# Optimization experiments

Hardware: AMD Instinct MI355X
Metric: run time of the kernel (lower is better)

The kernel has to match this reference:

```python
import jax, jax.numpy as jnp
import numpy as np
import math

B, C, HW = 4, 256, 32          # batch, seq_len (=channels), spatial side
D_MODEL = HW * HW              # 1024
OUT_C = 32 * 32                # 1024
D_STATE = 16
EXPAND = 2
D_INNER = EXPAND * D_MODEL     # 2048
DT_RANK = math.ceil(D_MODEL / 16)  # 64
D_CONV = 4


def setup_inputs() -> dict:
    key = jax.random.key(0)
    ks = jax.random.split(key, 12)
    s = 0.02
    x1 = jax.random.normal(ks[0], (B, C, HW, HW), dtype=jnp.float32)
    in_proj_w = jax.random.normal(ks[1], (2 * D_INNER, D_MODEL), dtype=jnp.float32) * s
    conv_w = jax.random.normal(ks[2], (D_INNER, 1, D_CONV), dtype=jnp.float32) * s
    conv_b = jnp.zeros((D_INNER,), dtype=jnp.float32)
    x_proj_w = jax.random.normal(ks[3], (DT_RANK + 2 * D_STATE, D_INNER), dtype=jnp.float32) * s
    dt_proj_w = jax.random.normal(ks[4], (D_INNER, DT_RANK), dtype=jnp.float32) * s
    dt_proj_b = jnp.zeros((D_INNER,), dtype=jnp.float32)
    A_log = jnp.log(jnp.broadcast_to(jnp.arange(1, D_STATE + 1, dtype=jnp.float32), (D_INNER, D_STATE)))
    D = jnp.ones((D_INNER,), dtype=jnp.float32)
    out_proj_w = jax.random.normal(ks[5], (OUT_C, D_INNER), dtype=jnp.float32) * s
    ln_w = jnp.ones((OUT_C,), dtype=jnp.float32)
    ln_b = jnp.zeros((OUT_C,), dtype=jnp.float32)
    return {"x1": x1, "in_proj_w": in_proj_w, "conv_w": conv_w, "conv_b": conv_b,
            "x_proj_w": x_proj_w, "dt_proj_w": dt_proj_w, "dt_proj_b": dt_proj_b,
            "A_log": A_log, "D": D, "out_proj_w": out_proj_w, "ln_w": ln_w, "ln_b": ln_b}


def _mamba_forward(x, in_proj_w, conv_w, conv_b, x_proj_w, dt_proj_w, dt_proj_b, A_log, D, out_proj_w):
    # x: (B, L, d_model)
    xz = jnp.einsum('bld,ed->ble', x, in_proj_w)            # (B,L,2*d_inner)
    xs, res = jnp.split(xz, 2, axis=-1)                     # each (B,L,d_inner)
    # depthwise causal conv1d, padding=d_conv-1 then truncate to L (== left pad)
    xs_c = jnp.transpose(xs, (0, 2, 1))                     # (B,d_inner,L)
    xs_c = jax.lax.conv_general_dilated(
        xs_c, conv_w, window_strides=(1,), padding=[(D_CONV - 1, 0)],
        dimension_numbers=('NCH', 'OIH', 'NCH'), feature_group_count=D_INNER)
    xs_c = xs_c + conv_b[None, :, None]
    xs = jax.nn.silu(jnp.transpose(xs_c, (0, 2, 1)))        # (B,L,d_inner)
    # input-dependent SSM parameters
    x_dbl = jnp.einsum('bld,ed->ble', xs, x_proj_w)         # (B,L,dt_rank+2N)
    dt, Bm, Cm = jnp.split(x_dbl, [DT_RANK, DT_RANK + D_STATE], axis=-1)
    delta = jax.nn.softplus(jnp.einsum('blr,dr->bld', dt, dt_proj_w) + dt_proj_b)  # (B,L,d_inner)
    A = -jnp.exp(A_log)                                     # (d_inner, N)
    deltaA = jnp.exp(delta[..., None] * A)                  # (B,L,d_inner,N)
    deltaB_u = delta[..., None] * Bm[:, :, None, :] * xs[..., None]  # (B,L,d_inner,N)

    def step(h, inp):
        dA, dBu, Ct = inp                                   # (B,d,N),(B,d,N),(B,N)
        h = dA * h + dBu
        y = jnp.einsum('bdn,bn->bd', h, Ct)
        return h, y

    h0 = jnp.zeros((deltaA.shape[0], D_INNER, D_STATE), dtype=deltaA.dtype)
    _, ys = jax.lax.scan(step, h0, (jnp.transpose(deltaA, (1, 0, 2, 3)),
                                    jnp.transpose(deltaB_u, (1, 0, 2, 3)),
                                    jnp.transpose(Cm, (1, 0, 2))))
    y = jnp.transpose(ys, (1, 0, 2))                        # (B,L,d_inner)
    y = y + D * xs
    y = y * jax.nn.silu(res)
    return jnp.einsum('bld,od->blo', y, out_proj_w)         # (B,L,out_c)


def reference(x1, in_proj_w, conv_w, conv_b, x_proj_w, dt_proj_w, dt_proj_b,
              A_log, D, out_proj_w, ln_w, ln_b):
    b, c, h, w = x1.shape
    x = x1.reshape(b, c, h * w)                             # (B, L=c, d_model)
    y = _mamba_forward(x, in_proj_w, conv_w, conv_b, x_proj_w, dt_proj_w,
                       dt_proj_b, A_log, D, out_proj_w)
    mu = jnp.mean(y, axis=-1, keepdims=True)
    var = jnp.var(y, axis=-1, keepdims=True)
    y = (y - mu) * jax.lax.rsqrt(var + 1e-5) * ln_w + ln_b
    return y.reshape(b, c, 32, 32)
```

## Files before the change

### kernel.cpp

```cpp
#include <hip/hip_runtime.h>
#include <hip/hip_bf16.h>
#include <math.h>

#define BATCH 4
#define SEQL 256
#define DMODEL 1024
#define DINNER 2048
#define DSTATE 16
#define DTRANK 64
#define OUTC 1024
#define NROWS (BATCH * SEQL)
#define NCHUNK 4
#define CH 64

typedef __attribute__((ext_vector_type(8))) short bf16x8;
typedef __attribute__((ext_vector_type(4))) float f32x4;

__global__ __launch_bounds__(256) void gemm_mfma(const __hip_bfloat16* __restrict__ A,
                                                 const __hip_bfloat16* __restrict__ B,
                                                 float* __restrict__ C,
                                                 int M, int N, int K,
                                                 int lda, int ldb) {
    __shared__ __hip_bfloat16 As[2][128 * 32];
    __shared__ __hip_bfloat16 Bs[2][128 * 32];
    const int t  = threadIdx.x;
    const int w  = t >> 6;
    const int ln = t & 63;
    const int wm = w >> 1, wn = w & 1;
    const int q  = ln >> 4, lr = ln & 15;
    const int m0 = blockIdx.y * 128;
    const int n0 = blockIdx.x * 128;
    const int Kpart = K / gridDim.z;
    const int kbase = blockIdx.z * Kpart;

    f32x4 acc[4][4] = {};

    const __hip_bfloat16* Ag = A + (size_t)m0 * lda + kbase;
    const __hip_bfloat16* Bg = B + (size_t)n0 * ldb + kbase;

    auto stage = [&](int k0, int buf) {
        #pragma unroll
        for (int i = 0; i < 2; ++i) {
            const int c = (i * 4 + w) * 64 + ln;
            const int r = c >> 2, col = (c & 3) * 8;
            __builtin_amdgcn_global_load_lds(
                (const __attribute__((address_space(1))) void*)(Ag + (size_t)r * lda + k0 + col),
                (__attribute__((address_space(3))) void*)(As[buf] + (i * 4 + w) * 64 * 8),
                16, 0, 0);
            __builtin_amdgcn_global_load_lds(
                (const __attribute__((address_space(1))) void*)(Bg + (size_t)r * ldb + k0 + col),
                (__attribute__((address_space(3))) void*)(Bs[buf] + (i * 4 + w) * 64 * 8),
                16, 0, 0);
        }
    };

    const int nk = Kpart / 32;
    stage(0, 0);
    __syncthreads();
    for (int kk = 0; kk < nk; ++kk) {
        if (kk + 1 < nk) stage((kk + 1) * 32, (kk + 1) & 1);
        const int buf = kk & 1;
        bf16x8 af[4], bfr[4];
        #pragma unroll
        for (int i = 0; i < 4; ++i)
            af[i] = *(const bf16x8*)(As[buf] + (wm * 64 + i * 16 + lr) * 32 + q * 8);
        #pragma unroll
        for (int j = 0; j < 4; ++j)
            bfr[j] = *(const bf16x8*)(Bs[buf] + (wn * 64 + j * 16 + lr) * 32 + q * 8);
        #pragma unroll
        for (int i = 0; i < 4; ++i)
            #pragma unroll
            for (int j = 0; j < 4; ++j)
                acc[i][j] = __builtin_amdgcn_mfma_f32_16x16x32_bf16(af[i], bfr[j], acc[i][j], 0, 0, 0);
        __syncthreads();
    }
    float* Cz = C + (size_t)blockIdx.z * M * N;
    #pragma unroll
    for (int i = 0; i < 4; ++i) {
        const int mrow = m0 + wm * 64 + i * 16 + q * 4;
        #pragma unroll
        for (int j = 0; j < 4; ++j) {
            const int ncol = n0 + wn * 64 + j * 16 + lr;
            #pragma unroll
            for (int r = 0; r < 4; ++r)
                Cz[(size_t)(mrow + r) * N + ncol] = acc[i][j][r];
        }
    }
}

__global__ __launch_bounds__(256) void gemm_dtsp(const __hip_bfloat16* __restrict__ A,
                                                 const __hip_bfloat16* __restrict__ B,
                                                 const float* __restrict__ bd,
                                                 float* __restrict__ delta) {
    __shared__ __hip_bfloat16 As[128 * 32];
    __shared__ __hip_bfloat16 Bs[128 * 32];
    const int t  = threadIdx.x;
    const int w  = t >> 6;
    const int ln = t & 63;
    const int wm = w >> 1, wn = w & 1;
    const int q  = ln >> 4, lr = ln & 15;
    const int m0 = blockIdx.y * 128;
    const int n0 = blockIdx.x * 128;
    const int lda = 128, ldb = 64, N = 2048;

    f32x4 acc[4][4] = {};
    const __hip_bfloat16* Ag = A + (size_t)m0 * lda;
    const __hip_bfloat16* Bg = B + (size_t)n0 * ldb;

    for (int k0 = 0; k0 < 64; k0 += 32) {
        #pragma unroll
        for (int i = 0; i < 2; ++i) {
            const int c = (i * 4 + w) * 64 + ln;
            const int r = c >> 2, col = (c & 3) * 8;
            __builtin_amdgcn_global_load_lds(
                (const __attribute__((address_space(1))) void*)(Ag + (size_t)r * lda + k0 + col),
                (__attribute__((address_space(3))) void*)(As + (i * 4 + w) * 64 * 8),
                16, 0, 0);
            __builtin_amdgcn_global_load_lds(
                (const __attribute__((address_space(1))) void*)(Bg + (size_t)r * ldb + k0 + col),
                (__attribute__((address_space(3))) void*)(Bs + (i * 4 + w) * 64 * 8),
                16, 0, 0);
        }
        __syncthreads();
        bf16x8 af[4], bfr[4];
        #pragma unroll
        for (int i = 0; i < 4; ++i)
            af[i] = *(const bf16x8*)(As + (wm * 64 + i * 16 + lr) * 32 + q * 8);
        #pragma unroll
        for (int j = 0; j < 4; ++j)
            bfr[j] = *(const bf16x8*)(Bs + (wn * 64 + j * 16 + lr) * 32 + q * 8);
        #pragma unroll
        for (int i = 0; i < 4; ++i)
            #pragma unroll
            for (int j = 0; j < 4; ++j)
                acc[i][j] = __builtin_amdgcn_mfma_f32_16x16x32_bf16(af[i], bfr[j], acc[i][j], 0, 0, 0);
        __syncthreads();
    }
    #pragma unroll
    for (int i = 0; i < 4; ++i) {
        const int mrow = m0 + wm * 64 + i * 16 + q * 4;
        #pragma unroll
        for (int j = 0; j < 4; ++j) {
            const int ncol = n0 + wn * 64 + j * 16 + lr;
            const float bias = bd[ncol];
            #pragma unroll
            for (int r = 0; r < 4; ++r) {
                float v = acc[i][j][r] + bias;
                float sp = (v > 20.f) ? v : log1pf(__expf(v));
                delta[(size_t)(mrow + r) * N + ncol] = sp;
            }
        }
    }
}

__global__ void xdbl_reduce_kernel(const float* __restrict__ part,
                                   float* __restrict__ xdbl,
                                   __hip_bfloat16* __restrict__ xdblb) {
    const int i = blockIdx.x * 256 + threadIdx.x;
    float s = 0.f;
    #pragma unroll
    for (int z = 0; z < 8; ++z) s += part[(size_t)z * (1024 * 128) + i];
    xdbl[i] = s;
    xdblb[i] = __float2bfloat16(s);
}

#define R0 (1024 * 1024)
#define R1 (R0 + 4096 * 1024)
#define R2 (R1 + 2048 * 1024)
#define R3 (R2 + 128 * 2048)
#define R4 (R3 + 2048 * 64)
__global__ void cast_all_kernel(const float* __restrict__ x1,
                                const float* __restrict__ w_in,
                                const float* __restrict__ w_out,
                                const float* __restrict__ w_xp,
                                const float* __restrict__ w_dt,
                                __hip_bfloat16* __restrict__ xa,
                                __hip_bfloat16* __restrict__ wb1,
                                __hip_bfloat16* __restrict__ wob,
                                __hip_bfloat16* __restrict__ wpb,
                                __hip_bfloat16* __restrict__ wdb) {
    int i = blockIdx.x * 256 + threadIdx.x;
    if (i < R0) {
        xa[i] = __float2bfloat16(x1[i]);
    } else if (i < R1) {
        int j = i - R0; wb1[j] = __float2bfloat16(w_in[j]);
    } else if (i < R2) {
        int j = i - R1; wob[j] = __float2bfloat16(w_out[j]);
    } else if (i < R3) {
        int j = i - R2; int e = j >> 11;
        wpb[j] = __float2bfloat16(e < 96 ? w_xp[j] : 0.f);
    } else if (i < R4) {
        int j = i - R3; wdb[j] = __float2bfloat16(w_dt[j]);
    }
}

__global__ void conv_silu_kernel(const float* __restrict__ xz,
                                 const float* __restrict__ conv_w,
                                 const float* __restrict__ conv_b,
                                 float* __restrict__ xs,
                                 __hip_bfloat16* __restrict__ xsb) {
    int idx = blockIdx.x * blockDim.x + threadIdx.x;
    int d = idx & (DINNER - 1);
    int l = (idx >> 11) & (SEQL - 1);
    int b = idx >> 19;
    const float w0 = conv_w[d * 4 + 0];
    const float w1 = conv_w[d * 4 + 1];
    const float w2 = conv_w[d * 4 + 2];
    const float w3 = conv_w[d * 4 + 3];
    float acc = conv_b[d];
    const size_t base = (size_t)(b * SEQL) * (2 * DINNER) + d;
    if (l >= 3) acc += w0 * xz[base + (size_t)(l - 3) * (2 * DINNER)];
    if (l >= 2) acc += w1 * xz[base + (size_t)(l - 2) * (2 * DINNER)];
    if (l >= 1) acc += w2 * xz[base + (size_t)(l - 1) * (2 * DINNER)];
    acc += w3 * xz[base + (size_t)l * (2 * DINNER)];
    float v = acc / (1.f + __expf(-acc));
    xs[idx] = v;
    xsb[idx] = __float2bfloat16(v);
}

__device__ __forceinline__ float row_reduce16(float x) {
    x += __int_as_float(__builtin_amdgcn_update_dpp(0, __float_as_int(x), 0x128, 0xF, 0xF, true));
    x += __int_as_float(__builtin_amdgcn_update_dpp(0, __float_as_int(x), 0x124, 0xF, 0xF, true));
    x += __int_as_float(__builtin_amdgcn_update_dpp(0, __float_as_int(x), 0x122, 0xF, 0xF, true));
    x += __int_as_float(__builtin_amdgcn_update_dpp(0, __float_as_int(x), 0x121, 0xF, 0xF, true));
    return x;
}

__global__ __launch_bounds__(256) void scan_carry_kernel(const float* __restrict__ delta,
                                                         const float* __restrict__ xs,
                                                         const float* __restrict__ xdbl,
                                                         const float* __restrict__ A_log,
                                                         float* __restrict__ carryL,
                                                         float* __restrict__ carryP) {
    __shared__ float sDU[CH][16][2];
    __shared__ float sB[CH][16];
    const int b = blockIdx.y, c = blockIdx.z, dg = blockIdx.x;
    const int t = threadIdx.x;
    const int dl = t >> 4, n = t & 15;
    const int d = dg * 16 + dl;
    const float a = -__expf(A_log[d * DSTATE + n]);
    const int srow = t >> 4, scol = t & 15;
    const int sd = dg * 16 + scol;
    const int rowbase = b * SEQL + c * CH;
    #pragma unroll
    for (int i = 0; i < 4; ++i) {
        const int row = rowbase + i * 16 + srow;
        const float dv = delta[(size_t)row * DINNER + sd];
        const float xv = xs[(size_t)row * DINNER + sd];
        sDU[i * 16 + srow][scol][0] = dv;
        sDU[i * 16 + srow][scol][1] = dv * xv;
        sB[i * 16 + srow][scol] = xdbl[row * 128 + 64 + scol];
    }
    __syncthreads();
    float h = 0.f, P = 1.f;
    #pragma unroll 16
    for (int l = 0; l < CH; ++l) {
        const float e = __expf(sDU[l][dl][0] * a);
        h = e * h + sDU[l][dl][1] * sB[l][n];
        P *= e;
    }
    const size_t ci = (((size_t)(b * NCHUNK + c)) * DINNER + d) * DSTATE + n;
    carryL[ci] = h;
    carryP[ci] = P;
}

__global__ __launch_bounds__(256) void scan_apply_kernel(const float* __restrict__ delta,
                                                         const float* __restrict__ xs,
                                                         const float* __restrict__ xdbl,
                                                         const float* __restrict__ xz,
                                                         const float* __restrict__ A_log,
                                                         const float* __restrict__ Dp,
                                                         const float* __restrict__ carryL,
                                                         const float* __restrict__ carryP,
                                                         __hip_bfloat16* __restrict__ ybb) {
    __shared__ float sDU[CH][16][2];
    __shared__ float sBC[CH][16][2];
    __shared__ float sGW[CH][16][2];
    const int b = blockIdx.y, c = blockIdx.z, dg = blockIdx.x;
    const int t = threadIdx.x;
    const int dl = t >> 4, n = t & 15;
    const int d = dg * 16 + dl;
    const float a = -__expf(A_log[d * DSTATE + n]);
    const int srow = t >> 4, scol = t & 15;
    const int sd = dg * 16 + scol;
    const float Dstage = Dp[sd];
    const int rowbase = b * SEQL + c * CH;
    #pragma unroll
    for (int i = 0; i < 4; ++i) {
        const int row = rowbase + i * 16 + srow;
        const float dv = delta[(size_t)row * DINNER + sd];
        const float xv = xs[(size_t)row * DINNER + sd];
        const float r  = xz[(size_t)row * (2 * DINNER) + DINNER + sd];
        const float g = r / (1.f + __expf(-r));
        const int lr_ = i * 16 + srow;
        sDU[lr_][scol][0] = dv;
        sDU[lr_][scol][1] = dv * xv;
        sGW[lr_][scol][0] = g;
        sGW[lr_][scol][1] = Dstage * xv * g;
        sBC[lr_][scol][0] = xdbl[row * 128 + 64 + scol];
        sBC[lr_][scol][1] = xdbl[row * 128 + 80 + scol];
    }
    __syncthreads();
    float h = 0.f;
    for (int j = 0; j < c; ++j) {
        const size_t ci = (((size_t)(b * NCHUNK + j)) * DINNER + d) * DSTATE + n;
        h = carryP[ci] * h + carryL[ci];
    }
    #pragma unroll 16
    for (int l = 0; l < CH; ++l) {
        const float e = __expf(sDU[l][dl][0] * a);
        h = e * h + sDU[l][dl][1] * sBC[l][n][0];
        float p = row_reduce16(h * sBC[l][n][1]);
        if (n == 0) {
            const float y = p * sGW[l][dl][0] + sGW[l][dl][1];
            ybb[(size_t)(rowbase + l) * DINNER + d] = __float2bfloat16(y);
        }
    }
}

__global__ __launch_bounds__(256) void ln_kernel(const float* __restrict__ opart,
                                                 const float* __restrict__ lw,
                                                 const float* __restrict__ lb,
                                                 float* __restrict__ out) {
    __shared__ float red[8];
    const int row = blockIdx.x;
    const int t = threadIdx.x;
    float v[4];
    float s = 0.f, s2 = 0.f;
    #pragma unroll
    for (int i = 0; i < 4; ++i) {
        const int c = t + 256 * i;
        float acc = 0.f;
        #pragma unroll
        for (int z = 0; z < 4; ++z)
            acc += opart[(size_t)z * (1024 * 1024) + (size_t)row * OUTC + c];
        v[i] = acc;
        s += acc;
        s2 += acc * acc;
    }
    #pragma unroll
    for (int o = 32; o; o >>= 1) {
        s += __shfl_down(s, o);
        s2 += __shfl_down(s2, o);
    }
    const int wid = t >> 6;
    if ((t & 63) == 0) { red[wid] = s; red[4 + wid] = s2; }
    __syncthreads();
    if (t == 0) {
        float ts = red[0] + red[1] + red[2] + red[3];
        float ts2 = red[4] + red[5] + red[6] + red[7];
        float mu = ts * (1.f / OUTC);
        float var = ts2 * (1.f / OUTC) - mu * mu;
        red[0] = mu;
        red[1] = rsqrtf(var + 1e-5f);
    }
    __syncthreads();
    const float mu = red[0], rs = red[1];
    #pragma unroll
    for (int i = 0; i < 4; ++i) {
        const int c = t + 256 * i;
        out[(size_t)row * OUTC + c] = (v[i] - mu) * rs * lw[c] + lb[c];
    }
}

extern "C" void kernel_launch(void* const* d_in, const int* in_sizes, int n_in,
                              void* d_out, int out_size, void* d_ws, size_t ws_size,
                              hipStream_t stream) {
    const float* x1        = (const float*)d_in[0];
    const float* in_proj_w = (const float*)d_in[1];
    const float* conv_w    = (const float*)d_in[2];
    const float* conv_b    = (const float*)d_in[3];
    const float* x_proj_w  = (const float*)d_in[4];
    const float* dt_proj_w = (const float*)d_in[5];
    const float* dt_proj_b = (const float*)d_in[6];
    const float* A_log     = (const float*)d_in[7];
    const float* Dp        = (const float*)d_in[8];
    const float* out_proj_w= (const float*)d_in[9];
    const float* ln_w      = (const float*)d_in[10];
    const float* ln_b      = (const float*)d_in[11];
    float* out = (float*)d_out;

    char* p = (char*)d_ws;
    __hip_bfloat16* xa    = (__hip_bfloat16*)p; p += (size_t)1024 * 1024 * 2;
    __hip_bfloat16* wb1   = (__hip_bfloat16*)p; p += (size_t)4096 * 1024 * 2;
    __hip_bfloat16* wpb   = (__hip_bfloat16*)p; p += (size_t)128 * 2048 * 2;
    __hip_bfloat16* wob   = (__hip_bfloat16*)p; p += (size_t)1024 * 2048 * 2;
    __hip_bfloat16* wdb   = (__hip_bfloat16*)p; p += (size_t)2048 * 64 * 2;
    __hip_bfloat16* xsb   = (__hip_bfloat16*)p; p += (size_t)1024 * 2048 * 2;
    __hip_bfloat16* ybb   = (__hip_bfloat16*)p; p += (size_t)1024 * 2048 * 2;
    __hip_bfloat16* xdblb = (__hip_bfloat16*)p; p += (size_t)1024 * 128 * 2;
    float* xz    = (float*)p; p += (size_t)1024 * 4096 * 4;
    float* xs    = (float*)p; p += (size_t)1024 * 2048 * 4;
    float* xdbl  = (float*)p; p += (size_t)1024 * 128 * 4;
    float* xpart = (float*)p; p += (size_t)8 * 1024 * 128 * 4;
    float* delta = (float*)p; p += (size_t)1024 * 2048 * 4;
    float* carryL = (float*)p; p += (size_t)BATCH * NCHUNK * DINNER * DSTATE * 4;
    float* carryP = (float*)p; p += (size_t)BATCH * NCHUNK * DINNER * DSTATE * 4;
    float* opart = xz;

    cast_all_kernel<<<(R4 + 255) / 256, 256, 0, stream>>>(x1, in_proj_w, out_proj_w,
                                                          x_proj_w, dt_proj_w,
                                                          xa, wb1, wob, wpb, wdb);
    gemm_mfma<<<dim3(32, 8, 1), 256, 0, stream>>>(xa, wb1, xz,
                                                  NROWS, 2 * DINNER, DMODEL, DMODEL, DMODEL);
    conv_silu_kernel<<<(NROWS * DINNER) / 256, 256, 0, stream>>>(xz, conv_w, conv_b, xs, xsb);
    gemm_mfma<<<dim3(1, 8, 8), 256, 0, stream>>>(xsb, wpb, xpart,
                                                 NROWS, 128, DINNER, DINNER, DINNER);
    xdbl_reduce_kernel<<<(1024 * 128) / 256, 256, 0, stream>>>(xpart, xdbl, xdblb);
    gemm_dtsp<<<dim3(16, 8), 256, 0, stream>>>(xdblb, wdb, dt_proj_b, delta);
    scan_carry_kernel<<<dim3(DINNER / 16, BATCH, NCHUNK), 256, 0, stream>>>(
        delta, xs, xdbl, A_log, carryL, carryP);
    scan_apply_kernel<<<dim3(DINNER / 16, BATCH, NCHUNK), 256, 0, stream>>>(
        delta, xs, xdbl, xz, A_log, Dp, carryL, carryP, ybb);
    gemm_mfma<<<dim3(8, 8, 4), 256, 0, stream>>>(ybb, wob, opart,
                                                 NROWS, OUTC, DINNER, DINNER, DINNER);
    ln_kernel<<<NROWS, 256, 0, stream>>>(opart, ln_w, ln_b, out);
}
```

Baseline: 219.6 us.

## Deepen GEMM LDS pipeline to four stages with vmcnt-based waits

The main MFMA GEMM now rotates through four LDS buffers and keeps three tiles in flight. It waits on explicit vmcnt counts plus a raw s_barrier instead of a full __syncthreads after every tile. The dt projection GEMM loads both of its K tiles up front and waits per tile, so the second load overlaps the first tile's math. This hides more global-to-LDS latency, at the cost of doubled LDS use, which can lower occupancy. The hand-counted vmcnt values also risk races if the compiler emits other memory ops in between.

```diff
diff --git a/kernel.cpp b/kernel.cpp
--- a/kernel.cpp
+++ b/kernel.cpp
@@ -21,8 +21,8 @@
                                                  float* __restrict__ C,
                                                  int M, int N, int K,
                                                  int lda, int ldb) {
-    __shared__ __hip_bfloat16 As[2][128 * 32];
-    __shared__ __hip_bfloat16 Bs[2][128 * 32];
+    __shared__ __hip_bfloat16 As[4][128 * 32];
+    __shared__ __hip_bfloat16 Bs[4][128 * 32];
     const int t  = threadIdx.x;
     const int w  = t >> 6;
     const int ln = t & 63;
@@ -55,11 +55,18 @@
     };
 
     const int nk = Kpart / 32;
-    stage(0, 0);
-    __syncthreads();
+    for (int s = 0; s < 3 && s < nk; ++s) stage(s * 32, s);
+
     for (int kk = 0; kk < nk; ++kk) {
-        if (kk + 1 < nk) stage((kk + 1) * 32, (kk + 1) & 1);
-        const int buf = kk & 1;
+        const int last = (kk + 2 < nk - 1) ? (kk + 2) : (nk - 1);
+        const int nf = last - kk;
+        if (nf >= 2)      asm volatile("s_waitcnt vmcnt(8)" ::: "memory");
+        else if (nf == 1) asm volatile("s_waitcnt vmcnt(4)" ::: "memory");
+        else              asm volatile("s_waitcnt vmcnt(0)" ::: "memory");
+        __builtin_amdgcn_s_barrier();
+        if (kk + 3 < nk) stage((kk + 3) * 32, (kk + 3) & 3);
+
+        const int buf = kk & 3;
         bf16x8 af[4], bfr[4];
         #pragma unroll
         for (int i = 0; i < 4; ++i)
@@ -72,7 +79,6 @@
             #pragma unroll
             for (int j = 0; j < 4; ++j)
                 acc[i][j] = __builtin_amdgcn_mfma_f32_16x16x32_bf16(af[i], bfr[j], acc[i][j], 0, 0, 0);
-        __syncthreads();
     }
     float* Cz = C + (size_t)blockIdx.z * M * N;
     #pragma unroll
@@ -92,8 +98,8 @@
                                                  const __hip_bfloat16* __restrict__ B,
                                                  const float* __restrict__ bd,
                                                  float* __restrict__ delta) {
-    __shared__ __hip_bfloat16 As[128 * 32];
-    __shared__ __hip_bfloat16 Bs[128 * 32];
+    __shared__ __hip_bfloat16 As[2][128 * 32];
+    __shared__ __hip_bfloat16 Bs[2][128 * 32];
     const int t  = threadIdx.x;
     const int w  = t >> 6;
     const int ln = t & 63;
@@ -107,34 +113,41 @@
     const __hip_bfloat16* Ag = A + (size_t)m0 * lda;
     const __hip_bfloat16* Bg = B + (size_t)n0 * ldb;
 
-    for (int k0 = 0; k0 < 64; k0 += 32) {
+    auto stage = [&](int k0, int buf) {
         #pragma unroll
         for (int i = 0; i < 2; ++i) {
             const int c = (i * 4 + w) * 64 + ln;
             const int r = c >> 2, col = (c & 3) * 8;
             __builtin_amdgcn_global_load_lds(
                 (const __attribute__((address_space(1))) void*)(Ag + (size_t)r * lda + k0 + col),
-                (__attribute__((address_space(3))) void*)(As + (i * 4 + w) * 64 * 8),
+                (__attribute__((address_space(3))) void*)(As[buf] + (i * 4 + w) * 64 * 8),
                 16, 0, 0);
             __builtin_amdgcn_global_load_lds(
                 (const __attribute__((address_space(1))) void*)(Bg + (size_t)r * ldb + k0 + col),
-                (__attribute__((address_space(3))) void*)(Bs + (i * 4 + w) * 64 * 8),
+                (__attribute__((address_space(3))) void*)(Bs[buf] + (i * 4 + w) * 64 * 8),
                 16, 0, 0);
         }
-        __syncthreads();
+    };
+
+    stage(0, 0);
+    stage(32, 1);
+    #pragma unroll
+    for (int kk = 0; kk < 2; ++kk) {
+        if (kk == 0) asm volatile("s_waitcnt vmcnt(4)" ::: "memory");
+        else         asm volatile("s_waitcnt vmcnt(0)" ::: "memory");
+        __builtin_amdgcn_s_barrier();
         bf16x8 af[4], bfr[4];
         #pragma unroll
         for (int i = 0; i < 4; ++i)
-            af[i] = *(const bf16x8*)(As + (wm * 64 + i * 16 + lr) * 32 + q * 8);
+            af[i] = *(const bf16x8*)(As[kk] + (wm * 64 + i * 16 + lr) * 32 + q * 8);
         #pragma unroll
         for (int j = 0; j < 4; ++j)
-            bfr[j] = *(const bf16x8*)(Bs + (wn * 64 + j * 16 + lr) * 32 + q * 8);
+            bfr[j] = *(const bf16x8*)(Bs[kk] + (wn * 64 + j * 16 + lr) * 32 + q * 8);
         #pragma unroll
         for (int i = 0; i < 4; ++i)
             #pragma unroll
             for (int j = 0; j < 4; ++j)
                 acc[i][j] = __builtin_amdgcn_mfma_f32_16x16x32_bf16(af[i], bfr[j], acc[i][j], 0, 0, 0);
-        __syncthreads();
     }
     #pragma unroll
     for (int i = 0; i < 4; ++i) {
```

After: 220.0 us. Within noise of the previous version (+0.2%).
